# Performance work log

Hardware: AMD Instinct MI355X
Metric: run time of the kernel (lower is better)

Reference implementation:

```python
import jax, jax.numpy as jnp
import numpy as np


def setup_inputs() -> dict:
    key = jax.random.key(0)
    k1, k2, k3, k4 = jax.random.split(key, 4)
    return {
        "src_feat1": jax.random.normal(k1, (4, 1024, 64, 64), dtype=jnp.float32),
        "tar_feat1": jax.random.normal(k2, (4, 1024, 64, 64), dtype=jnp.float32),
        "src_feat2": jax.random.normal(k3, (4, 2048, 32, 32), dtype=jnp.float32),
        "tar_feat2": jax.random.normal(k4, (4, 2048, 32, 32), dtype=jnp.float32),
    }


def _nn_concat(src, tar):
    # src: [B,C,H1,W1], tar: [B,C,H2,W2] -> [B,2C,H1,W1]
    B, C, H, W = src.shape
    s = src.reshape(B, C, -1).transpose(0, 2, 1)   # [B,N1,C]
    t = tar.reshape(B, C, -1).transpose(0, 2, 1)   # [B,N2,C]
    # squared euclidean distance (argmin of d^2 == argmin of d, sqrt monotonic)
    d2 = (
        jnp.sum(s * s, axis=-1, keepdims=True)      # [B,N1,1]
        + jnp.sum(t * t, axis=-1)[:, None, :]       # [B,1,N2]
        - 2.0 * jnp.einsum("bnc,bmc->bnm", s, t)    # [B,N1,N2]
    )
    idx = jnp.argmin(d2, axis=2)                    # [B,N1]
    nearest = jnp.take_along_axis(t, idx[..., None], axis=1)  # [B,N1,C]
    nearest = nearest.transpose(0, 2, 1).reshape(B, C, H, W)
    return jnp.concatenate([src, nearest], axis=1)


def reference(src_feat1, tar_feat1, src_feat2, tar_feat2):
    c1 = _nn_concat(src_feat1, tar_feat1)           # [B,2048,64,64]
    c2 = _nn_concat(src_feat2, tar_feat2)           # [B,4096,32,32]
    B, C2 = c2.shape[:2]
    H1, W1 = c1.shape[2], c1.shape[3]
    # F.interpolate(mode='bilinear', align_corners=False) == jax.image.resize 'linear'
    c2r = jax.image.resize(c2, (B, C2, H1, W1), method="linear")
    return jnp.concatenate([c1, c2r], axis=1)       # [B,6144,64,64]
```

## Files before the change

### kernel.cpp

```cpp
#include <hip/hip_runtime.h>
#include <cstdint>

using u8 = unsigned char;
using u64 = unsigned long long;

typedef _Float16 f16x8 __attribute__((ext_vector_type(8)));
typedef float f32x4 __attribute__((ext_vector_type(4)));
typedef unsigned short u16x8 __attribute__((ext_vector_type(8)));

__device__ __forceinline__ void gload16(const void* g, void* l) {
  __builtin_amdgcn_global_load_lds((const __attribute__((address_space(1))) void*)g,
                                   (__attribute__((address_space(3))) void*)l, 16, 0, 0);
}

#define VMCNT(N) asm volatile("s_waitcnt vmcnt(" #N ")" ::: "memory")

__device__ __forceinline__ void split_body(const float* __restrict__ in,
                                           _Float16* __restrict__ hi,
                                           _Float16* __restrict__ lo,
                                           float* __restrict__ hnp,
                                           int C, int N, int NC,
                                           int cblk, int nblk, int b, bool with_hn) {
  const int n = nblk * 256 + (int)threadIdx.x;
  const int c0 = cblk * 32;
  const float* inB = in + (size_t)b * C * N;
  f16x8 hv[4], lv[4];
  float ss = 0.f;
#pragma unroll
  for (int g = 0; g < 4; ++g)
#pragma unroll
    for (int e = 0; e < 8; ++e) {
      float x = inB[(size_t)(c0 + g * 8 + e) * N + n];
      _Float16 h = (_Float16)x;
      float r = (x - (float)h) * 4096.f;
      hv[g][e] = h;
      lv[g][e] = (_Float16)r;
      ss = fmaf(x, x, ss);
    }
  _Float16* oh = hi + ((size_t)b * N + n) * C + c0;
  _Float16* ol = lo + ((size_t)b * N + n) * C + c0;
#pragma unroll
  for (int g = 0; g < 4; ++g) {
    *(f16x8*)(oh + g * 8) = hv[g];
    *(f16x8*)(ol + g * 8) = lv[g];
  }
  if (with_hn) hnp[((size_t)b * NC + cblk) * N + n] = ss;
}

__global__ __launch_bounds__(256) void prep_all(
    const float* __restrict__ s1, const float* __restrict__ t1,
    const float* __restrict__ s2, const float* __restrict__ t2,
    _Float16* __restrict__ h1s, _Float16* __restrict__ l1s,
    _Float16* __restrict__ h1t, _Float16* __restrict__ l1t,
    _Float16* __restrict__ h2s, _Float16* __restrict__ l2s,
    _Float16* __restrict__ h2t, _Float16* __restrict__ l2t,
    float* __restrict__ hnp1, float* __restrict__ hnp2) {
  const int f = (int)blockIdx.x;
  if (f < 4096) {
    const bool isT = f >= 2048;
    const int local = f & 2047;
    const int cblk = local & 31;
    const int r = local >> 5;
    const int nblk = r & 15, b = r >> 4;
    split_body(isT ? t1 : s1, isT ? h1t : h1s, isT ? l1t : l1s, hnp1,
               1024, 4096, 32, cblk, nblk, b, isT);
  } else {
    const int l0 = f - 4096;
    const bool isT = l0 >= 1024;
    const int local = l0 & 1023;
    const int cblk = local & 63;
    const int r = local >> 6;
    const int nblk = r & 3, b = r >> 2;
    split_body(isT ? t2 : s2, isT ? h2t : h2s, isT ? l2t : l2s, hnp2,
               2048, 1024, 64, cblk, nblk, b, isT);
  }
}

__global__ __launch_bounds__(256) void hn_all(const float* __restrict__ hnp1,
                                              const float* __restrict__ hnp2,
                                              float* __restrict__ hn1,
                                              float* __restrict__ hn2) {
  const int x = (int)blockIdx.x, b = (int)blockIdx.y;
  if (x < 16) {
    const int n = x * 256 + (int)threadIdx.x;
    float a = 0.f;
    for (int cc = 0; cc < 32; ++cc) a += hnp1[((size_t)b * 32 + cc) * 4096 + n];
    hn1[(size_t)b * 4096 + n] = 0.5f * a;
  } else {
    const int n = (x - 16) * 256 + (int)threadIdx.x;
    float a = 0.f;
    for (int cc = 0; cc < 64; ++cc) a += hnp2[((size_t)b * 64 + cc) * 1024 + n];
    hn2[(size_t)b * 1024 + n] = 0.5f * a;
  }
}

#define MFMA_BLOCK(GI)                                                         \
  __builtin_amdgcn_s_barrier();                                                \
  asm volatile("s_waitcnt lgkmcnt(0)" ::: "memory");                           \
  __builtin_amdgcn_sched_barrier(0);                                           \
  __builtin_amdgcn_s_setprio(1);                                               \
  _Pragma("unroll") for (int i2 = 0; i2 < 4; ++i2)                             \
      _Pragma("unroll") for (int j = 0; j < NJ; ++j) acc[(GI)*4 + i2][j] =     \
      __builtin_amdgcn_mfma_f32_16x16x32_f16(av[i2], bv[j],                    \
                                             acc[(GI)*4 + i2][j], 0, 0, 0);    \
  __builtin_amdgcn_s_setprio(0);                                               \
  asm volatile("" ::: "memory");                                               \
  __builtin_amdgcn_s_barrier();

template <int MI, int NJ, int WCN, int NTH>
__global__ __launch_bounds__(NTH, 2) void nn_filter8(
    const u8* __restrict__ Ahi, const u8* __restrict__ Bhi,
    const float* __restrict__ hn, unsigned short* __restrict__ sc,
    int M, int N, int NT , int mBlocks, int nBlocks) {
  constexpr int BM = 2 * MI * 16;
  constexpr int G = MI / 4;
  constexpr int CHUNK_A = BM * 64;
  constexpr int CHUNK = 2 * CHUNK_A;
  __shared__ u8 smem[4 * CHUNK];

  const int tid = threadIdx.x;
  const int lane = tid & 63;
  const int wid = tid >> 6;
  const int wrow = wid / WCN;
  const int wcol = wid % WCN;
  const int lr = lane & 15, kh = lane >> 4;

  const int cpx = (int)gridDim.x >> 3;
  const int bid = (int)blockIdx.x;
  const int sbid = (bid & 7) * cpx + (bid >> 3);
  const int perB = mBlocks * nBlocks;
  const int b = sbid / perB;
  const int rr = sbid - b * perB;
  const int n1 = rr & 3;
  const int t2 = rr >> 2;
  const int mb = t2 % mBlocks;
  const int n2 = t2 / mBlocks;
  const int mbase = mb * BM;
  const int nbase = (n2 * 4 + n1) * BM;
  const size_t rstride = (size_t)NT * 128;

  const int r0 = (tid >> 6) * 16 + ((tid & 63) >> 2);
  const int sA = ((lane & 3) ^ (r0 >> 1)) & 3;
  const u8* aP0 = Ahi + ((size_t)b * M + mbase + r0) * rstride + sA * 16;
  const u8* aP1 = aP0 + (size_t)(NTH / 4) * rstride;
  const u8* bP0 = Bhi + ((size_t)b * N + nbase + r0) * rstride + sA * 16;
  const u8* bP1 = bP0 + (size_t)(NTH / 4) * rstride;

  auto STAGE = [&](int X, int h) {
    const size_t ko = (size_t)X * 128 + h * 64;
    u8* cb = smem + ((X & 1) * 2 + h) * CHUNK;
    gload16(aP0 + ko, cb + tid * 16);
    gload16(aP1 + ko, cb + NTH * 16 + tid * 16);
    gload16(bP0 + ko, cb + CHUNK_A + tid * 16);
    gload16(bP1 + ko, cb + CHUNK_A + NTH * 16 + tid * 16);
  };

  int a_off[MI], b_off[NJ];
#pragma unroll
  for (int i = 0; i < MI; ++i) {
    const int row = wrow * (MI * 16) + i * 16 + lr;
    a_off[i] = row * 64 + (((kh ^ (row >> 1)) & 3) << 4);
  }
#pragma unroll
  for (int j = 0; j < NJ; ++j) {
    const int row = wcol * (NJ * 16) + j * 16 + lr;
    b_off[j] = CHUNK_A + row * 64 + (((kh ^ (row >> 1)) & 3) << 4);
  }

  f32x4 acc[MI][NJ];
#pragma unroll
  for (int i = 0; i < MI; ++i)
#pragma unroll
    for (int j = 0; j < NJ; ++j) acc[i][j] = f32x4{0.f, 0.f, 0.f, 0.f};

  STAGE(0, 0);
  STAGE(0, 1);
  STAGE(1, 0);
  VMCNT(8);
  __builtin_amdgcn_s_barrier();

  for (int X = 0; X < NT; ++X) {
    const u8* cb0 = smem + ((X & 1) * 2) * CHUNK;
    const u8* cb1 = cb0 + CHUNK;
    f16x8 av[4], bv[NJ];

#pragma unroll
    for (int j = 0; j < NJ; ++j) bv[j] = *(const f16x8*)(cb0 + b_off[j]);
#pragma unroll
    for (int i2 = 0; i2 < 4; ++i2) av[i2] = *(const f16x8*)(cb0 + a_off[i2]);
    if (X + 1 < NT) STAGE(X + 1, 1);
    if (X + 1 < NT) { VMCNT(8); } else { VMCNT(0); }
    MFMA_BLOCK(0)

    if constexpr (G == 2) {
#pragma unroll
      for (int i2 = 0; i2 < 4; ++i2) av[i2] = *(const f16x8*)(cb0 + a_off[4 + i2]);
      MFMA_BLOCK(1)
    }

#pragma unroll
    for (int j = 0; j < NJ; ++j) bv[j] = *(const f16x8*)(cb1 + b_off[j]);
#pragma unroll
    for (int i2 = 0; i2 < 4; ++i2) av[i2] = *(const f16x8*)(cb1 + a_off[i2]);
    if (X + 2 < NT) STAGE(X + 2, 0);
    if (X + 1 < NT) {
      if (X + 2 < NT) { VMCNT(8); } else { VMCNT(4); }
    }
    MFMA_BLOCK(0)

    if constexpr (G == 2) {
#pragma unroll
      for (int i2 = 0; i2 < 4; ++i2) av[i2] = *(const f16x8*)(cb1 + a_off[4 + i2]);
      MFMA_BLOCK(1)
    }
  }

  const float* hnB = hn + (size_t)b * N;
  float hnv[NJ];
  int ncol[NJ];
#pragma unroll
  for (int j = 0; j < NJ; ++j) {
    ncol[j] = nbase + wcol * (NJ * 16) + j * 16 + lr;
    hnv[j] = hnB[ncol[j]];
  }
  unsigned short* scB = sc + (size_t)b * M * N;
#pragma unroll
  for (int i = 0; i < MI; ++i)
#pragma unroll
    for (int r = 0; r < 4; ++r) {
      const int m = mbase + wrow * (MI * 16) + i * 16 + kh * 4 + r;
      unsigned short* srow = scB + (size_t)m * N;
#pragma unroll
      for (int j = 0; j < NJ; ++j) {
        float score = hnv[j] - acc[i][j][r];
        int qi = (int)(score * 64.0f);
        qi = qi < 0 ? 0 : (qi > 65535 ? 65535 : qi);
        srow[ncol[j]] = (unsigned short)qi;
      }
    }
}

template <int K, int CH>
__global__ __launch_bounds__(256) void select_rescore(
    const unsigned short* __restrict__ sc,
    const _Float16* __restrict__ hiA, const _Float16* __restrict__ loA,
    const _Float16* __restrict__ hiB, const _Float16* __restrict__ loB,
    const float* __restrict__ hn, unsigned* __restrict__ idx, int M, int N) {
  const int w = threadIdx.x >> 6, lane = threadIdx.x & 63;
  const int row = blockIdx.x * 4 + w;
  const int b = blockIdx.y;
  const unsigned short* q = sc + ((size_t)b * M + row) * N;

  unsigned cm[CH];
#pragma unroll
  for (int ch = 0; ch < CH; ++ch) {
    u16x8 v = *(const u16x8*)(q + ch * 512 + lane * 8);
    unsigned m0 = v[0] < v[1] ? v[0] : v[1];
    unsigned m1 = v[2] < v[3] ? v[2] : v[3];
    unsigned m2 = v[4] < v[5] ? v[4] : v[5];
    unsigned m3 = v[6] < v[7] ? v[6] : v[7];
    m0 = m0 < m1 ? m0 : m1;
    m2 = m2 < m3 ? m2 : m3;
    unsigned m = m0 < m2 ? m0 : m2;
#pragma unroll
    for (int off = 32; off >= 1; off >>= 1) {
      unsigned o = (unsigned)__shfl_xor((int)m, off);
      m = o < m ? o : m;
    }
    cm[ch] = m;
  }
  unsigned mn = 0xFFFFu;
#pragma unroll
  for (int ch = 0; ch < CH; ++ch) mn = cm[ch] < mn ? cm[ch] : mn;
  const unsigned thr = mn + 64;

  constexpr int PER = K / 64;
  const float inv = 2.44140625e-4f;
  float sv[PER];
  const _Float16* hA = hiA + ((size_t)b * M + row) * K;
  const _Float16* lA = loA + ((size_t)b * M + row) * K;
#pragma unroll
  for (int i = 0; i < PER; ++i)
    sv[i] = fmaf((float)lA[i * 64 + lane], inv, (float)hA[i * 64 + lane]);

  float bestv = 3.4e38f;
  int bestn = 0x7FFFFFFF;
  const float* hnB = hn + (size_t)b * N;
#pragma unroll
  for (int ch = 0; ch < CH; ++ch) {
    if (cm[ch] > thr) continue;
    u16x8 v = *(const u16x8*)(q + ch * 512 + lane * 8);
#pragma unroll
    for (int e = 0; e < 8; ++e) {
      u64 mask = __ballot((unsigned)v[e] <= thr);
      while (mask) {
        int bit = __ffsll((long long)mask) - 1;
        mask &= mask - 1;
        int n = ch * 512 + bit * 8 + e;
        const _Float16* hB = hiB + ((size_t)b * N + n) * K;
        const _Float16* lB = loB + ((size_t)b * N + n) * K;
        float part = 0.f;
#pragma unroll
        for (int i = 0; i < PER; ++i)
          part = fmaf(sv[i], fmaf((float)lB[i * 64 + lane], inv, (float)hB[i * 64 + lane]), part);
#pragma unroll
        for (int off = 32; off >= 1; off >>= 1) part += __shfl_xor(part, off);
        float scf = hnB[n] - part;
        if (scf < bestv || (scf == bestv && n < bestn)) { bestv = scf; bestn = n; }
      }
    }
  }
  if (lane == 0) idx[(size_t)b * M + row] = (unsigned)bestn;
}

__global__ __launch_bounds__(256) void finalize(
    const float* __restrict__ src1, const float* __restrict__ tar1,
    const float* __restrict__ src2, const float* __restrict__ tar2,
    const unsigned* __restrict__ idx1, const unsigned* __restrict__ idx2,
    float* __restrict__ out) {
  const int b = blockIdx.y;
  int c = (int)blockIdx.x;
  if (c < 2048) {
    float* orow = out + ((size_t)b * 6144 + c) * 4096;
    if (c < 1024) {
      const float4* s4 = (const float4*)(src1 + ((size_t)b * 1024 + c) * 4096);
      float4* o4 = (float4*)orow;
#pragma unroll
      for (int i = 0; i < 4; ++i) o4[threadIdx.x + i * 256] = s4[threadIdx.x + i * 256];
    } else {
      const float* trow = tar1 + ((size_t)b * 1024 + (c - 1024)) * 4096;
      const unsigned* ib = idx1 + (size_t)b * 4096;
      for (int p = threadIdx.x; p < 4096; p += 256) orow[p] = trow[ib[p]];
    }
    return;
  }
  c -= 2048;
  __shared__ float row[1024];
  if (c < 2048) {
    const float* in = src2 + ((size_t)b * 2048 + c) * 1024;
    for (int p = threadIdx.x; p < 1024; p += 256) row[p] = in[p];
  } else {
    const float* trow = tar2 + ((size_t)b * 2048 + (c - 2048)) * 1024;
    const unsigned* ib = idx2 + (size_t)b * 1024;
    for (int p = threadIdx.x; p < 1024; p += 256) row[p] = trow[ib[p]];
  }
  __syncthreads();
  float* orow = out + ((size_t)b * 6144 + 2048 + c) * 4096;
  for (int q = threadIdx.x; q < 4096; q += 256) {
    int y = q >> 6, x = q & 63;
    int ky = y >> 1, kx = x >> 1;
    int y0, y1, x0, x1;
    float wy0, wy1, wx0, wx1;
    if (y & 1) { y0 = ky; y1 = (ky + 1 < 32) ? ky + 1 : 31; wy0 = 0.75f; wy1 = 0.25f; }
    else       { y0 = (ky > 0) ? ky - 1 : 0; y1 = ky;       wy0 = 0.25f; wy1 = 0.75f; }
    if (x & 1) { x0 = kx; x1 = (kx + 1 < 32) ? kx + 1 : 31; wx0 = 0.75f; wx1 = 0.25f; }
    else       { x0 = (kx > 0) ? kx - 1 : 0; x1 = kx;       wx0 = 0.25f; wx1 = 0.75f; }
    float v = wy0 * (wx0 * row[y0 * 32 + x0] + wx1 * row[y0 * 32 + x1]) +
              wy1 * (wx0 * row[y1 * 32 + x0] + wx1 * row[y1 * 32 + x1]);
    orow[q] = v;
  }
}

extern "C" void kernel_launch(void* const* d_in, const int* in_sizes, int n_in,
                              void* d_out, int out_size, void* d_ws, size_t ws_size,
                              hipStream_t stream) {
  const float* src1 = (const float*)d_in[0];
  const float* tar1 = (const float*)d_in[1];
  const float* src2 = (const float*)d_in[2];
  const float* tar2 = (const float*)d_in[3];
  float* out = (float*)d_out;

  u8* scratch = (u8*)d_out;
  _Float16* hi1s = (_Float16*)scratch;
  _Float16* lo1s = (_Float16*)(scratch + (32ull << 20));
  _Float16* hi1t = (_Float16*)(scratch + (64ull << 20));
  _Float16* lo1t = (_Float16*)(scratch + (96ull << 20));
  _Float16* hi2s = (_Float16*)(scratch + (128ull << 20));
  _Float16* lo2s = (_Float16*)(scratch + (144ull << 20));
  _Float16* hi2t = (_Float16*)(scratch + (160ull << 20));
  _Float16* lo2t = (_Float16*)(scratch + (176ull << 20));
  unsigned short* sc1 = (unsigned short*)(scratch + (192ull << 20));
  unsigned short* sc2 = (unsigned short*)(scratch + (320ull << 20));
  float* hnp1 = (float*)(scratch + (328ull << 20));
  float* hnp2 = (float*)(scratch + (331ull << 20));

  float* hn1 = (float*)d_ws;
  float* hn2 = hn1 + 4 * 4096;
  unsigned* idx1 = (unsigned*)(hn2 + 4 * 1024);
  unsigned* idx2 = idx1 + 4 * 4096;

  prep_all<<<6144, 256, 0, stream>>>(src1, tar1, src2, tar2,
                                     hi1s, lo1s, hi1t, lo1t,
                                     hi2s, lo2s, hi2t, lo2t, hnp1, hnp2);
  hn_all<<<dim3(20, 4), 256, 0, stream>>>(hnp1, hnp2, hn1, hn2);

  nn_filter8<8, 4, 4, 512><<<1024, 512, 0, stream>>>(
      (const u8*)hi1s, (const u8*)hi1t, hn1, sc1, 4096, 4096, 16, 16, 16);
  nn_filter8<4, 4, 2, 256><<<256, 256, 0, stream>>>(
      (const u8*)hi2s, (const u8*)hi2t, hn2, sc2, 1024, 1024, 32, 8, 8);

  select_rescore<1024, 8><<<dim3(1024, 4), 256, 0, stream>>>(
      sc1, hi1s, lo1s, hi1t, lo1t, hn1, idx1, 4096, 4096);
  select_rescore<2048, 2><<<dim3(256, 4), 256, 0, stream>>>(
      sc2, hi2s, lo2s, hi2t, lo2t, hn2, idx2, 1024, 1024);

  finalize<<<dim3(6144, 4), 256, 0, stream>>>(src1, tar1, src2, tar2, idx1, idx2, out);
}
```

Before: 558.9 us.

## Merge both scale filter and select launches into single grouped kernels

```diff
diff --git a/kernel.cpp b/kernel.cpp
--- a/kernel.cpp
+++ b/kernel.cpp
@@ -107,36 +107,22 @@
   asm volatile("" ::: "memory");                                               \
   __builtin_amdgcn_s_barrier();
 
-template <int MI, int NJ, int WCN, int NTH>
-__global__ __launch_bounds__(NTH, 2) void nn_filter8(
+__device__ __forceinline__ void filter_body(
     const u8* __restrict__ Ahi, const u8* __restrict__ Bhi,
     const float* __restrict__ hn, unsigned short* __restrict__ sc,
-    int M, int N, int NT , int mBlocks, int nBlocks) {
-  constexpr int BM = 2 * MI * 16;
-  constexpr int G = MI / 4;
+    int M, int N, int NT, int mbase, int nbase, int b, u8* smem) {
+  constexpr int MI = 8, NJ = 4;
+  constexpr int BM = 256;
   constexpr int CHUNK_A = BM * 64;
   constexpr int CHUNK = 2 * CHUNK_A;
-  __shared__ u8 smem[4 * CHUNK];
+  constexpr int NTH = 512;
 
   const int tid = threadIdx.x;
   const int lane = tid & 63;
   const int wid = tid >> 6;
-  const int wrow = wid / WCN;
-  const int wcol = wid % WCN;
+  const int wrow = wid >> 2;
+  const int wcol = wid & 3;
   const int lr = lane & 15, kh = lane >> 4;
-
-  const int cpx = (int)gridDim.x >> 3;
-  const int bid = (int)blockIdx.x;
-  const int sbid = (bid & 7) * cpx + (bid >> 3);
-  const int perB = mBlocks * nBlocks;
-  const int b = sbid / perB;
-  const int rr = sbid - b * perB;
-  const int n1 = rr & 3;
-  const int t2 = rr >> 2;
-  const int mb = t2 % mBlocks;
-  const int n2 = t2 / mBlocks;
-  const int mbase = mb * BM;
-  const int nbase = (n2 * 4 + n1) * BM;
   const size_t rstride = (size_t)NT * 128;
 
   const int r0 = (tid >> 6) * 16 + ((tid & 63) >> 2);
@@ -192,11 +178,9 @@
     if (X + 1 < NT) { VMCNT(8); } else { VMCNT(0); }
     MFMA_BLOCK(0)
 
-    if constexpr (G == 2) {
-#pragma unroll
-      for (int i2 = 0; i2 < 4; ++i2) av[i2] = *(const f16x8*)(cb0 + a_off[4 + i2]);
-      MFMA_BLOCK(1)
-    }
+#pragma unroll
+    for (int i2 = 0; i2 < 4; ++i2) av[i2] = *(const f16x8*)(cb0 + a_off[4 + i2]);
+    MFMA_BLOCK(1)
 
 #pragma unroll
     for (int j = 0; j < NJ; ++j) bv[j] = *(const f16x8*)(cb1 + b_off[j]);
@@ -208,11 +192,9 @@
     }
     MFMA_BLOCK(0)
 
-    if constexpr (G == 2) {
-#pragma unroll
-      for (int i2 = 0; i2 < 4; ++i2) av[i2] = *(const f16x8*)(cb1 + a_off[4 + i2]);
-      MFMA_BLOCK(1)
-    }
+#pragma unroll
+    for (int i2 = 0; i2 < 4; ++i2) av[i2] = *(const f16x8*)(cb1 + a_off[4 + i2]);
+    MFMA_BLOCK(1)
   }
 
   const float* hnB = hn + (size_t)b * N;
@@ -240,15 +222,43 @@
     }
 }
 
+__global__ __launch_bounds__(512, 2) void nn_filter_all(
+    const u8* __restrict__ A1, const u8* __restrict__ B1,
+    const float* __restrict__ hn1, unsigned short* __restrict__ sc1,
+    const u8* __restrict__ A2, const u8* __restrict__ B2,
+    const float* __restrict__ hn2, unsigned short* __restrict__ sc2) {
+  __shared__ u8 smem[4 * 32768];
+  const int bid = (int)blockIdx.x;
+  if (bid < 64) {
+    const int sbid = (bid & 7) * 8 + (bid >> 3);
+    const int b = sbid >> 4;
+    const int rr = sbid & 15;
+    const int n1 = rr & 3;
+    const int mb = rr >> 2;
+    filter_body(A2, B2, hn2, sc2, 1024, 1024, 32, mb * 256, n1 * 256, b, smem);
+  } else {
+    const int l = bid - 64;
+    const int sbid = (l & 7) * 128 + (l >> 3);
+    const int perB = 256;
+    const int b = sbid / perB;
+    const int rr = sbid - b * perB;
+    const int n1 = rr & 3;
+    const int t2 = rr >> 2;
+    const int mb = t2 & 15;
+    const int n2 = t2 >> 4;
+    filter_body(A1, B1, hn1, sc1, 4096, 4096, 16, mb * 256, (n2 * 4 + n1) * 256, b, smem);
+  }
+}
+
 template <int K, int CH>
-__global__ __launch_bounds__(256) void select_rescore(
+__device__ __forceinline__ void select_body(
     const unsigned short* __restrict__ sc,
     const _Float16* __restrict__ hiA, const _Float16* __restrict__ loA,
     const _Float16* __restrict__ hiB, const _Float16* __restrict__ loB,
-    const float* __restrict__ hn, unsigned* __restrict__ idx, int M, int N) {
+    const float* __restrict__ hn, unsigned* __restrict__ idx,
+    int M, int N, int rowblk, int b) {
   const int w = threadIdx.x >> 6, lane = threadIdx.x & 63;
-  const int row = blockIdx.x * 4 + w;
-  const int b = blockIdx.y;
+  const int row = rowblk * 4 + w;
   const unsigned short* q = sc + ((size_t)b * M + row) * N;
 
   unsigned cm[CH];
@@ -311,6 +321,22 @@
     }
   }
   if (lane == 0) idx[(size_t)b * M + row] = (unsigned)bestn;
+}
+
+__global__ __launch_bounds__(256) void select_all(
+    const unsigned short* __restrict__ sc1,
+    const _Float16* __restrict__ h1s, const _Float16* __restrict__ l1s,
+    const _Float16* __restrict__ h1t, const _Float16* __restrict__ l1t,
+    const float* __restrict__ hn1, unsigned* __restrict__ idx1,
+    const unsigned short* __restrict__ sc2,
+    const _Float16* __restrict__ h2s, const _Float16* __restrict__ l2s,
+    const _Float16* __restrict__ h2t, const _Float16* __restrict__ l2t,
+    const float* __restrict__ hn2, unsigned* __restrict__ idx2) {
+  const int x = (int)blockIdx.x, b = (int)blockIdx.y;
+  if (x < 1024)
+    select_body<1024, 8>(sc1, h1s, l1s, h1t, l1t, hn1, idx1, 4096, 4096, x, b);
+  else
+    select_body<2048, 2>(sc2, h2s, l2s, h2t, l2t, hn2, idx2, 1024, 1024, x - 1024, b);
 }
 
 __global__ __launch_bounds__(256) void finalize(
@@ -394,15 +420,13 @@
                                      hi2s, lo2s, hi2t, lo2t, hnp1, hnp2);
   hn_all<<<dim3(20, 4), 256, 0, stream>>>(hnp1, hnp2, hn1, hn2);
 
-  nn_filter8<8, 4, 4, 512><<<1024, 512, 0, stream>>>(
-      (const u8*)hi1s, (const u8*)hi1t, hn1, sc1, 4096, 4096, 16, 16, 16);
-  nn_filter8<4, 4, 2, 256><<<256, 256, 0, stream>>>(
-      (const u8*)hi2s, (const u8*)hi2t, hn2, sc2, 1024, 1024, 32, 8, 8);
-
-  select_rescore<1024, 8><<<dim3(1024, 4), 256, 0, stream>>>(
-      sc1, hi1s, lo1s, hi1t, lo1t, hn1, idx1, 4096, 4096);
-  select_rescore<2048, 2><<<dim3(256, 4), 256, 0, stream>>>(
-      sc2, hi2s, lo2s, hi2t, lo2t, hn2, idx2, 1024, 1024);
+  nn_filter_all<<<1088, 512, 0, stream>>>(
+      (const u8*)hi1s, (const u8*)hi1t, hn1, sc1,
+      (const u8*)hi2s, (const u8*)hi2t, hn2, sc2);
+
+  select_all<<<dim3(1280, 4), 256, 0, stream>>>(
+      sc1, hi1s, lo1s, hi1t, lo1t, hn1, idx1,
+      sc2, hi2s, lo2s, hi2t, lo2t, hn2, idx2);
 
   finalize<<<dim3(6144, 4), 256, 0, stream>>>(src1, tar1, src2, tar2, idx1, idx2, out);
 }
```

Result: faster. 536.1 us (-4.1%).
